# Performance work log

Hardware: AMD Instinct MI355X
Metric: run time of the kernel (lower is better)

## Reference

```python
import jax, jax.numpy as jnp
import numpy as np

G, NB, C, K, R, S = 5, 5, 64, 3, 8, 2   # n_groups, n_blocks, n_feats, kernel, reduction, scale
MOCO = 256


def setup_inputs() -> dict:
    key = jax.random.key(0)
    ks = iter(jax.random.split(key, 32))
    def rn(shape, s=0.02):
        return jax.random.normal(next(ks), shape, jnp.float32) * s
    return {
        "x": jax.random.normal(next(ks), (16, 3, 64, 64), jnp.float32),
        "k_v": jax.random.normal(next(ks), (16, MOCO), jnp.float32),
        "head_w": rn((C, 3, K, K)), "head_b": rn((C,)),
        "comp_w": rn((C, MOCO)),
        # DA_conv params, stacked over [group, block, which-of-2]
        "da_kw1": rn((G, NB, 2, C, C)),
        "da_kw2": rn((G, NB, 2, C * K * K, C)),
        "da_cw": rn((G, NB, 2, C, C)), "da_cb": rn((G, NB, 2, C)),
        "ca_w1": rn((G, NB, 2, C // R, C)), "ca_w2": rn((G, NB, 2, C, C // R)),
        # DAB plain 3x3 convs (conv1, conv2)
        "dab_cw": rn((G, NB, 2, C, C, K, K)), "dab_cb": rn((G, NB, 2, C)),
        # per-group tail conv, body tail conv, upsampler, final conv
        "grp_w": rn((G, C, C, K, K)), "grp_b": rn((G, C)),
        "body_w": rn((C, C, K, K)), "body_b": rn((C,)),
        "up_w": rn((C * S * S, C, K, K)), "up_b": rn((C * S * S,)),
        "tail_w": rn((3, C, K, K)), "tail_b": rn((3,)),
    }


def lrelu(x):
    return jax.nn.leaky_relu(x, 0.1)


def conv2d(x, w, b):
    p = (K - 1) // 2
    y = jax.lax.conv_general_dilated(x, w, (1, 1), [(p, p), (p, p)],
                                     dimension_numbers=("NCHW", "OIHW", "NCHW"))
    return y + b[None, :, None, None]


def da_conv(x, kv, kw1, kw2, cw, cb, caw1, caw2):
    # x: [B,C,H,W], kv: [B,C]
    B, Ch, H, W = x.shape
    # per-sample, per-channel dynamic KxK kernel (torch: groups=B*C depthwise conv)
    ker = (lrelu(kv @ kw1.T) @ kw2.T).reshape(B, Ch, K, K)
    p = (K - 1) // 2
    xp = jnp.pad(x, ((0, 0), (0, 0), (p, p), (p, p)))
    out = jnp.zeros_like(x)
    for i in range(K):
        for j in range(K):
            out = out + ker[:, :, i, j, None, None] * xp[:, :, i:i + H, j:j + W]
    out = lrelu(out)
    # 1x1 conv (with bias)
    out = jnp.einsum("bchw,oc->bohw", out, cw) + cb[None, :, None, None]
    # CA gate on kv (two bias-free 1x1 convs on 1x1 spatial == matmuls)
    att = jax.nn.sigmoid(lrelu(kv @ caw1.T) @ caw2.T)  # [B,C]
    return out + x * att[:, :, None, None]


def pixel_shuffle(t, r):
    B, Ct, H, W = t.shape
    c = Ct // (r * r)
    return t.reshape(B, c, r, r, H, W).transpose(0, 1, 4, 2, 5, 3).reshape(B, c, H * r, W * r)


def _forward(x, k_v, head_w, head_b, comp_w, da_kw1, da_kw2, da_cw, da_cb,
             ca_w1, ca_w2, dab_cw, dab_cb, grp_w, grp_b, body_w, body_b,
             up_w, up_b, tail_w, tail_b):
    kv = lrelu(k_v @ comp_w.T)            # compress: [B, C]
    x0 = conv2d(x, head_w, head_b)        # head
    res = x0
    for g in range(G):                    # DAGs
        gin = res
        for n in range(NB):               # DABs
            bin_ = res
            out = lrelu(da_conv(res, kv, da_kw1[g, n, 0], da_kw2[g, n, 0],
                                da_cw[g, n, 0], da_cb[g, n, 0], ca_w1[g, n, 0], ca_w2[g, n, 0]))
            out = lrelu(conv2d(out, dab_cw[g, n, 0], dab_cb[g, n, 0]))
            out = lrelu(da_conv(out, kv, da_kw1[g, n, 1], da_kw2[g, n, 1],
                                da_cw[g, n, 1], da_cb[g, n, 1], ca_w1[g, n, 1], ca_w2[g, n, 1]))
            res = conv2d(out, dab_cw[g, n, 1], dab_cb[g, n, 1]) + bin_
        res = conv2d(res, grp_w[g], grp_b[g]) + gin
    res = conv2d(res, body_w, body_b) + x0
    t = pixel_shuffle(conv2d(res, up_w, up_b), S)   # Upsampler (scale=2)
    return conv2d(t, tail_w, tail_b)


def reference(x, k_v, head_w, head_b, comp_w, da_kw1, da_kw2, da_cw, da_cb,
              ca_w1, ca_w2, dab_cw, dab_cb, grp_w, grp_b, body_w, body_b,
              up_w, up_b, tail_w, tail_b):
    return _forward(x, k_v, head_w, head_b, comp_w, da_kw1, da_kw2, da_cw, da_cb,
                    ca_w1, ca_w2, dab_cw, dab_cb, grp_w, grp_b, body_w, body_b,
                    up_w, up_b, tail_w, tail_b)
```

## Files before the change

### kernel.cpp

```cpp
#include <hip/hip_runtime.h>
#include <math.h>

#define DEV __device__ __forceinline__

DEV float lrelu_f(float v) { return v > 0.f ? v : 0.1f * v; }

DEV unsigned short f2bf(float f) {
    unsigned u = __builtin_bit_cast(unsigned, f);
    unsigned r = u + 0x7FFFu + ((u >> 16) & 1u);
    return (unsigned short)(r >> 16);
}

DEV float bf2f(unsigned short s) {
    return __builtin_bit_cast(float, (unsigned)s << 16);
}

typedef __attribute__((ext_vector_type(8))) short bh8;
typedef __attribute__((ext_vector_type(16))) float f16acc;

#define MFMA32(acc, a, b) acc = __builtin_amdgcn_mfma_f32_32x32x16_bf16(a, b, acc, 0, 0, 0)

__global__ void transpose_w(const float* __restrict__ src, float* __restrict__ dst,
                            int L, int O, int KK) {
    int idx = blockIdx.x * 256 + threadIdx.x;
    int tot = L * O * KK;
    if (idx >= tot) return;
    int l = idx / (O * KK);
    int r = idx - l * (O * KK);
    int o = r / KK;
    int k = r - o * KK;
    dst[((size_t)l * KK + k) * O + o] = src[idx];
}

__global__ void pack3x3(const float* __restrict__ src, unsigned short* __restrict__ dst, int L) {
    int idx = blockIdx.x * 256 + threadIdx.x;
    if (idx >= L * 4608) return;
    int l = idx / 4608;
    int r = idx - l * 4608;
    int c = r >> 7;
    int rr = r & 127;
    int nt = rr >> 6, lane = rr & 63;
    int o = nt * 32 + (lane & 31);
    int kg = lane >> 5;
    unsigned short v[8];
#pragma unroll
    for (int j = 0; j < 8; ++j) {
        int k = c * 16 + kg * 8 + j;
        int t = k >> 6, cin = k & 63;
        v[j] = f2bf(src[(((size_t)l * 64 + o) * 64 + cin) * 9 + t]);
    }
    uint4 u;
    u.x = v[0] | ((unsigned)v[1] << 16);
    u.y = v[2] | ((unsigned)v[3] << 16);
    u.z = v[4] | ((unsigned)v[5] << 16);
    u.w = v[6] | ((unsigned)v[7] << 16);
    *(uint4*)(dst + (size_t)idx * 8) = u;
}

__global__ void pack_da(const float* __restrict__ src, unsigned short* __restrict__ dst, int L) {
    int idx = blockIdx.x * 256 + threadIdx.x;
    if (idx >= L * 512) return;
    int l = idx >> 9;
    int r = idx & 511;
    int c = r >> 7;
    int rr = r & 127;
    int nt = rr >> 6, lane = rr & 63;
    int o = nt * 32 + (lane & 31);
    int kg = lane >> 5;
    unsigned short v[8];
#pragma unroll
    for (int j = 0; j < 8; ++j) {
        int cin = c * 16 + kg * 8 + j;
        v[j] = f2bf(src[((size_t)l * 64 + o) * 64 + cin]);
    }
    uint4 u;
    u.x = v[0] | ((unsigned)v[1] << 16);
    u.y = v[2] | ((unsigned)v[3] << 16);
    u.z = v[4] | ((unsigned)v[5] << 16);
    u.w = v[6] | ((unsigned)v[7] << 16);
    *(uint4*)(dst + (size_t)idx * 8) = u;
}

__global__ void pack_up(const float* __restrict__ src, unsigned short* __restrict__ dst) {
    int idx = blockIdx.x * 256 + threadIdx.x;
    if (idx >= 18432) return;
    int c = idx >> 9;
    int nt = (idx >> 6) & 7;
    int lane = idx & 63;
    int o = nt * 32 + (lane & 31);
    int kg = lane >> 5;
    unsigned short v[8];
#pragma unroll
    for (int j = 0; j < 8; ++j) {
        int k = c * 16 + kg * 8 + j;
        int t = k >> 6, cin = k & 63;
        v[j] = f2bf(src[((size_t)o * 64 + cin) * 9 + t]);
    }
    uint4 u;
    u.x = v[0] | ((unsigned)v[1] << 16);
    u.y = v[2] | ((unsigned)v[3] << 16);
    u.z = v[4] | ((unsigned)v[5] << 16);
    u.w = v[6] | ((unsigned)v[7] << 16);
    *(uint4*)(dst + (size_t)idx * 8) = u;
}

__global__ void pack_tail(const float* __restrict__ src, unsigned short* __restrict__ dst) {
    int idx = blockIdx.x * 256 + threadIdx.x;
    if (idx >= 2304) return;
    int c = idx >> 6;
    int lane = idx & 63;
    int o = lane & 31;
    int kg = lane >> 5;
    unsigned short v[8];
#pragma unroll
    for (int j = 0; j < 8; ++j) {
        int k = c * 16 + kg * 8 + j;
        int t = k >> 6, cin = k & 63;
        v[j] = (o < 3) ? f2bf(src[((size_t)o * 64 + cin) * 9 + t]) : (unsigned short)0;
    }
    uint4 u;
    u.x = v[0] | ((unsigned)v[1] << 16);
    u.y = v[2] | ((unsigned)v[3] << 16);
    u.z = v[4] | ((unsigned)v[5] << 16);
    u.w = v[6] | ((unsigned)v[7] << 16);
    *(uint4*)(dst + (size_t)idx * 8) = u;
}

__global__ void kv_kernel(const float* __restrict__ kvin, const float* __restrict__ comp_w,
                          float* __restrict__ kv) {
    int b = blockIdx.x, c = threadIdx.x;
    const float* a = kvin + b * 256;
    const float* w = comp_w + c * 256;
    float s = 0.f;
    for (int m = 0; m < 256; ++m) s += a[m] * w[m];
    kv[b * 64 + c] = lrelu_f(s);
}

__global__ void kerprep(const float* __restrict__ kv, const float* __restrict__ kw1,
                        const float* __restrict__ kw2, const float* __restrict__ caw1,
                        const float* __restrict__ caw2, float* __restrict__ ker_all,
                        float* __restrict__ att_all) {
    int l = blockIdx.x >> 4;
    int b = blockIdx.x & 15;
    int c = threadIdx.x;
    __shared__ float kvb[64];
    __shared__ float t1[64];
    __shared__ float a1[8];
    kvb[c] = kv[b * 64 + c];
    __syncthreads();
    {
        const float* w1 = kw1 + (size_t)l * 4096 + c * 64;
        float s = 0.f;
        for (int j = 0; j < 64; ++j) s += kvb[j] * w1[j];
        t1[c] = lrelu_f(s);
    }
    if (c < 8) {
        const float* cw1 = caw1 + (size_t)l * 512 + c * 64;
        float s = 0.f;
        for (int j = 0; j < 64; ++j) s += kvb[j] * cw1[j];
        a1[c] = lrelu_f(s);
    }
    __syncthreads();
    const float* w2 = kw2 + (size_t)l * 576 * 64;
    for (int t = 0; t < 9; ++t) {
        const float* row = w2 + (size_t)(c * 9 + t) * 64;
        float s = 0.f;
        for (int j = 0; j < 64; ++j) s += t1[j] * row[j];
        ker_all[(((size_t)l * 16 + b) * 9 + t) * 64 + c] = s;
    }
    {
        const float* c2 = caw2 + (size_t)l * 512 + c * 8;
        float s = 0.f;
        for (int r = 0; r < 8; ++r) s += a1[r] * c2[r];
        att_all[((size_t)l * 16 + b) * 64 + c] = 1.f / (1.f + expf(-s));
    }
}

__global__ __launch_bounds__(256) void head_conv(const float* __restrict__ x,
                                                 const float* __restrict__ wt,
                                                 const float* __restrict__ bias,
                                                 float* __restrict__ x0,
                                                 float* __restrict__ res,
                                                 unsigned short* __restrict__ resS) {
    int t = threadIdx.x;
    int co = t & 63, q = t >> 6;
    int bid = blockIdx.x;
    int b = bid >> 7;
    int rem = bid & 127;
    int y = rem >> 1;
    int xs = (rem & 1) * 32 + q * 8;

    float bv = bias[co];
    float acc[8];
#pragma unroll
    for (int p = 0; p < 8; ++p) acc[p] = bv;

    int coff[10];
    bool cok[10];
#pragma unroll
    for (int i = 0; i < 10; ++i) {
        int col = xs - 1 + i;
        cok[i] = (col >= 0) && (col < 64);
        coff[i] = cok[i] ? col : 0;
    }
    for (int cin = 0; cin < 3; ++cin) {
#pragma unroll
        for (int ky = 0; ky < 3; ++ky) {
            int row = y + ky - 1;
            bool rok = (row >= 0) && (row < 64);
            const float* rp = x + ((size_t)(b * 3 + cin) * 64 + (rok ? row : 0)) * 64;
            float v[10];
#pragma unroll
            for (int i = 0; i < 10; ++i) v[i] = (rok && cok[i]) ? rp[coff[i]] : 0.f;
            const float* wp = wt + ((cin * 3 + ky) * 3) * 64 + co;
            float w0 = wp[0], w1 = wp[64], w2 = wp[128];
#pragma unroll
            for (int p = 0; p < 8; ++p) acc[p] += w0 * v[p] + w1 * v[p + 1] + w2 * v[p + 2];
        }
    }
    size_t ob = (((size_t)b * 64 + y) * 64 + xs) * 64 + co;
#pragma unroll
    for (int p = 0; p < 8; ++p) {
        x0[ob + (size_t)p * 64] = acc[p];
        res[ob + (size_t)p * 64] = acc[p];
        resS[ob + (size_t)p * 64] = f2bf(acc[p]);
    }
}

__global__ __launch_bounds__(256, 2) void conv3x3_mfma(const unsigned short* __restrict__ in,
                                                       const unsigned short* __restrict__ wp,
                                                       const float* __restrict__ bias,
                                                       const float* __restrict__ residF,
                                                       float* __restrict__ outF,
                                                       unsigned short* __restrict__ outB,
                                                       int act) {
    __shared__ unsigned short sm[180 * 72];
    int tid = threadIdx.x;
    int bid = blockIdx.x;
    int b = bid >> 5;
    int rem = bid & 31;
    int ty = rem >> 2, tx = rem & 3;
    const unsigned short* inb = in + (size_t)b * 262144;

    int lane = tid & 63, w = tid >> 6;
    const unsigned short* bp = wp + (size_t)lane * 8;

    bh8 q0[6], q1[6];
#pragma unroll
    for (int i = 0; i < 6; ++i) {
        q0[i] = *(const bh8*)&bp[(size_t)i * 1024];
        q1[i] = *(const bh8*)&bp[(size_t)i * 1024 + 512];
    }

    for (int i = tid; i < 1440; i += 256) {
        int px = i >> 3, c8 = i & 7;
        int hy = px / 18, hx = px - hy * 18;
        int row = ty * 8 + hy - 1, col = tx * 16 + hx - 1;
        uint4 u = make_uint4(0u, 0u, 0u, 0u);
        if (row >= 0 && row < 64 && col >= 0 && col < 64)
            u = *(const uint4*)(inb + (((size_t)row * 64 + col) * 64 + c8 * 8));
        *(uint4*)&sm[px * 72 + c8 * 8] = u;
    }
    __syncthreads();

    int l31 = lane & 31, kg8 = (lane >> 5) * 8, hi = lane >> 5;
    int p0 = w * 32 + l31;
    int ly0 = p0 >> 4, lx0 = p0 & 15;

    f16acc a0 = {0,0,0,0,0,0,0,0,0,0,0,0,0,0,0,0};
    f16acc a1 = a0;

#pragma unroll
    for (int c = 0; c < 36; ++c) {
        int t = c >> 2, cc = c & 3;
        int tyt = t / 3, txt = t - tyt * 3;
        int base = ((ly0 + tyt) * 18 + lx0 + txt) * 72 + cc * 16 + kg8;
        bh8 A = *(const bh8*)&sm[base];
        bh8 B0 = q0[c % 6], B1 = q1[c % 6];
        if (c + 6 < 36) {
            q0[c % 6] = *(const bh8*)&bp[(size_t)(c + 6) * 1024];
            q1[c % 6] = *(const bh8*)&bp[(size_t)(c + 6) * 1024 + 512];
        }
        MFMA32(a0, A, B0);
        MFMA32(a1, A, B1);
    }

    float bias0 = bias[l31], bias1 = bias[32 + l31];
    size_t outb = (size_t)b * 262144;
#pragma unroll
    for (int r = 0; r < 16; ++r) {
        int rowm = (r & 3) + 8 * (r >> 2) + 4 * hi;
        int m = w * 32 + rowm;
        int gy = ty * 8 + (m >> 4), gx = tx * 16 + (m & 15);
        size_t i0 = outb + (((size_t)gy * 64 + gx) * 64);
        float v0 = a0[r] + bias0, v1 = a1[r] + bias1;
        if (residF) {
            v0 += residF[i0 + l31];
            v1 += residF[i0 + 32 + l31];
        }
        if (act) { v0 = lrelu_f(v0); v1 = lrelu_f(v1); }
        if (outF) {
            outF[i0 + l31] = v0;
            outF[i0 + 32 + l31] = v1;
        }
        if (outB) {
            outB[i0 + l31] = f2bf(v0);
            outB[i0 + 32 + l31] = f2bf(v1);
        }
    }
}

__global__ __launch_bounds__(256, 2) void dab_mfma(const unsigned short* __restrict__ in,
                                                   const unsigned short* __restrict__ wda,
                                                   const float* __restrict__ cb,
                                                   const float* __restrict__ kerT,
                                                   const float* __restrict__ attv,
                                                   const unsigned short* __restrict__ wconv,
                                                   const float* __restrict__ cbias,
                                                   const float* __restrict__ residF,
                                                   float* __restrict__ outF,
                                                   unsigned short* __restrict__ outB,
                                                   int act) {
    __shared__ unsigned short sin_[240 * 72];
    __shared__ unsigned short mid[192 * 72];
    int tid = threadIdx.x;
    int bid = blockIdx.x;
    int b = bid >> 5;
    int rem = bid & 31;
    int ty = rem >> 2, tx = rem & 3;
    const unsigned short* inb = in + (size_t)b * 262144;

    int lane = tid & 63, w = tid >> 6;
    int l31 = lane & 31, kg8 = (lane >> 5) * 8, hi = lane >> 5;

    bh8 dB0[4], dB1[4];
#pragma unroll
    for (int cc = 0; cc < 4; ++cc) {
        dB0[cc] = *(const bh8*)&wda[((size_t)(cc * 2 + 0) * 64 + lane) * 8];
        dB1[cc] = *(const bh8*)&wda[((size_t)(cc * 2 + 1) * 64 + lane) * 8];
    }

    for (int i = tid; i < 1920; i += 256) {
        int px = i >> 3, c8 = i & 7;
        int hy = px / 20, hx = px - hy * 20;
        int row = ty * 8 + hy - 2, col = tx * 16 + hx - 2;
        uint4 u = make_uint4(0u, 0u, 0u, 0u);
        if (row >= 0 && row < 64 && col >= 0 && col < 64)
            u = *(const uint4*)(inb + (((size_t)row * 64 + col) * 64 + c8 * 8));
        *(uint4*)&sin_[px * 72 + c8 * 8] = u;
    }
    __syncthreads();

    {
        int c2 = tid & 31, q = tid >> 5;
        const float* kb = kerT + (size_t)b * 576 + 2 * c2;
        float ka[9], kbv[9];
#pragma unroll
        for (int t = 0; t < 9; ++t) {
            ka[t] = kb[t * 64];
            kbv[t] = kb[t * 64 + 1];
        }
#pragma unroll
        for (int rr = 0; rr < 2; ++rr) {
            int my = (rr == 0) ? q : 8 + q;
            if (rr == 1 && q >= 2) break;
            float m0[18], m1[18];
#pragma unroll
            for (int xx = 0; xx < 18; ++xx) { m0[xx] = 0.f; m1[xx] = 0.f; }
#pragma unroll
            for (int ky = 0; ky < 3; ++ky) {
                int sr = my + ky;
                float va[20], vb[20];
#pragma unroll
                for (int i = 0; i < 20; ++i) {
                    unsigned u = *(const unsigned*)&sin_[(sr * 20 + i) * 72 + 2 * c2];
                    va[i] = bf2f((unsigned short)(u & 0xffffu));
                    vb[i] = bf2f((unsigned short)(u >> 16));
                }
                float k0a = ka[ky * 3], k1a = ka[ky * 3 + 1], k2a = ka[ky * 3 + 2];
                float k0b = kbv[ky * 3], k1b = kbv[ky * 3 + 1], k2b = kbv[ky * 3 + 2];
#pragma unroll
                for (int xx = 0; xx < 18; ++xx) {
                    m0[xx] += k0a * va[xx] + k1a * va[xx + 1] + k2a * va[xx + 2];
                    m1[xx] += k0b * vb[xx] + k1b * vb[xx + 1] + k2b * vb[xx + 2];
                }
            }
#pragma unroll
            for (int xx = 0; xx < 18; ++xx) {
                int px = my * 18 + xx;
                unsigned u = (unsigned)f2bf(lrelu_f(m0[xx])) |
                             ((unsigned)f2bf(lrelu_f(m1[xx])) << 16);
                *(unsigned*)&mid[px * 72 + 2 * c2] = u;
            }
        }
    }
    __syncthreads();

    {
        float cb0 = cb[l31], cb1 = cb[32 + l31];
        float at0 = attv[b * 64 + l31], at1 = attv[b * 64 + 32 + l31];
        for (int mt = w; mt < 6; mt += 4) {
            f16acc a0 = {0,0,0,0,0,0,0,0,0,0,0,0,0,0,0,0};
            f16acc a1 = a0;
#pragma unroll
            for (int cc = 0; cc < 4; ++cc) {
                bh8 A = *(const bh8*)&mid[(mt * 32 + l31) * 72 + cc * 16 + kg8];
                MFMA32(a0, A, dB0[cc]);
                MFMA32(a1, A, dB1[cc]);
            }
#pragma unroll
            for (int r = 0; r < 16; ++r) {
                int rowm = (r & 3) + 8 * (r >> 2) + 4 * hi;
                int px = mt * 32 + rowm;
                if (px < 180) {
                    int my = px / 18, mx = px - my * 18;
                    int gy = ty * 8 + my - 1, gx = tx * 16 + mx - 1;
                    bool ok = (gy >= 0) && (gy < 64) && (gx >= 0) && (gx < 64);
                    int spx = (my + 1) * 20 + (mx + 1);
                    float i0v = bf2f(sin_[spx * 72 + l31]);
                    float i1v = bf2f(sin_[spx * 72 + 32 + l31]);
                    float v0 = lrelu_f(a0[r] + cb0 + i0v * at0);
                    float v1 = lrelu_f(a1[r] + cb1 + i1v * at1);
                    mid[px * 72 + l31] = ok ? f2bf(v0) : (unsigned short)0;
                    mid[px * 72 + 32 + l31] = ok ? f2bf(v1) : (unsigned short)0;
                }
            }
        }
    }

    const unsigned short* bp = wconv + (size_t)lane * 8;
    bh8 q0[6], q1[6];
#pragma unroll
    for (int i = 0; i < 6; ++i) {
        q0[i] = *(const bh8*)&bp[(size_t)i * 1024];
        q1[i] = *(const bh8*)&bp[(size_t)i * 1024 + 512];
    }
    __syncthreads();

    int p0 = w * 32 + l31;
    int ly0 = p0 >> 4, lx0 = p0 & 15;

    f16acc c0 = {0,0,0,0,0,0,0,0,0,0,0,0,0,0,0,0};
    f16acc c1 = c0;

#pragma unroll
    for (int c = 0; c < 36; ++c) {
        int t = c >> 2, cc = c & 3;
        int tyt = t / 3, txt = t - tyt * 3;
        int base = ((ly0 + tyt) * 18 + lx0 + txt) * 72 + cc * 16 + kg8;
        bh8 A = *(const bh8*)&mid[base];
        bh8 B0 = q0[c % 6], B1 = q1[c % 6];
        if (c + 6 < 36) {
            q0[c % 6] = *(const bh8*)&bp[(size_t)(c + 6) * 1024];
            q1[c % 6] = *(const bh8*)&bp[(size_t)(c + 6) * 1024 + 512];
        }
        MFMA32(c0, A, B0);
        MFMA32(c1, A, B1);
    }

    float bias0 = cbias[l31], bias1 = cbias[32 + l31];
    size_t outb = (size_t)b * 262144;
#pragma unroll
    for (int r = 0; r < 16; ++r) {
        int rowm = (r & 3) + 8 * (r >> 2) + 4 * hi;
        int m = w * 32 + rowm;
        int gy = ty * 8 + (m >> 4), gx = tx * 16 + (m & 15);
        size_t i0 = outb + (((size_t)gy * 64 + gx) * 64);
        float v0 = c0[r] + bias0, v1 = c1[r] + bias1;
        if (residF) {
            v0 += residF[i0 + l31];
            v1 += residF[i0 + 32 + l31];
        }
        if (act) { v0 = lrelu_f(v0); v1 = lrelu_f(v1); }
        if (outF) {
            outF[i0 + l31] = v0;
            outF[i0 + 32 + l31] = v1;
        }
        if (outB) {
            outB[i0 + l31] = f2bf(v0);
            outB[i0 + 32 + l31] = f2bf(v1);
        }
    }
}

__global__ __launch_bounds__(256, 2) void up_mfma(const unsigned short* __restrict__ in,
                                                  const unsigned short* __restrict__ wp,
                                                  const float* __restrict__ bias,
                                                  unsigned short* __restrict__ shuf) {
    __shared__ unsigned short sm[100 * 72];
    int tid = threadIdx.x;
    int bid = blockIdx.x;
    int b = bid >> 6;
    int t6 = bid & 63;
    int ty = t6 >> 3, tx = t6 & 7;
    const unsigned short* inb = in + (size_t)b * 262144;

    int lane = tid & 63, w = tid >> 6;
    const unsigned short* bp = wp + (size_t)(w * 2) * 512 + (size_t)lane * 8;

    bh8 q0[4], q1[4];
#pragma unroll
    for (int i = 0; i < 4; ++i) {
        q0[i] = *(const bh8*)&bp[(size_t)i * 4096];
        q1[i] = *(const bh8*)&bp[(size_t)i * 4096 + 512];
    }

    for (int i = tid; i < 800; i += 256) {
        int px = i >> 3, c8 = i & 7;
        int hy = px / 10, hx = px - hy * 10;
        int row = ty * 8 + hy - 1, col = tx * 8 + hx - 1;
        uint4 u = make_uint4(0u, 0u, 0u, 0u);
        if (row >= 0 && row < 64 && col >= 0 && col < 64)
            u = *(const uint4*)(inb + (((size_t)row * 64 + col) * 64 + c8 * 8));
        *(uint4*)&sm[px * 72 + c8 * 8] = u;
    }
    __syncthreads();

    int l31 = lane & 31, kg8 = (lane >> 5) * 8, hi = lane >> 5;
    int ly0 = l31 >> 3, lx0 = l31 & 7;

    f16acc a00 = {0,0,0,0,0,0,0,0,0,0,0,0,0,0,0,0};
    f16acc a01 = a00, a10 = a00, a11 = a00;

#pragma unroll
    for (int c = 0; c < 36; ++c) {
        int t = c >> 2, cc = c & 3;
        int tyt = t / 3, txt = t - tyt * 3;
        int base0 = ((ly0 + tyt) * 10 + lx0 + txt) * 72 + cc * 16 + kg8;
        int base1 = base0 + 2880;
        bh8 A0 = *(const bh8*)&sm[base0];
        bh8 A1 = *(const bh8*)&sm[base1];
        bh8 B0 = q0[c % 4], B1 = q1[c % 4];
        if (c + 4 < 36) {
            q0[c % 4] = *(const bh8*)&bp[(size_t)(c + 4) * 4096];
            q1[c % 4] = *(const bh8*)&bp[(size_t)(c + 4) * 4096 + 512];
        }
        MFMA32(a00, A0, B0);
        MFMA32(a01, A0, B1);
        MFMA32(a10, A1, B0);
        MFMA32(a11, A1, B1);
    }

    int co0 = w * 64 + l31, co1 = co0 + 32;
    float bias0 = bias[co0], bias1 = bias[co1];
    int ch0 = co0 >> 2, r10 = (co0 >> 1) & 1, r20 = co0 & 1;
    int ch1 = co1 >> 2, r11 = (co1 >> 1) & 1, r21 = co1 & 1;
#pragma unroll
    for (int r = 0; r < 16; ++r) {
        int rowm = (r & 3) + 8 * (r >> 2) + 4 * hi;
#pragma unroll
        for (int mt = 0; mt < 2; ++mt) {
            int m = mt * 32 + rowm;
            int y = ty * 8 + (m >> 3), x = tx * 8 + (m & 7);
            float va = (mt == 0) ? a00[r] : a10[r];
            float vb = (mt == 0) ? a01[r] : a11[r];
            shuf[(((size_t)b * 128 + 2 * y + r10) * 128 + 2 * x + r20) * 64 + ch0] = f2bf(va + bias0);
            shuf[(((size_t)b * 128 + 2 * y + r11) * 128 + 2 * x + r21) * 64 + ch1] = f2bf(vb + bias1);
        }
    }
}

__global__ __launch_bounds__(256) void tail_mfma(const unsigned short* __restrict__ shuf,
                                                 const unsigned short* __restrict__ wp,
                                                 const float* __restrict__ bias,
                                                 float* __restrict__ outp) {
    __shared__ unsigned short sm[324 * 72];
    int tid = threadIdx.x;
    int bid = blockIdx.x;
    int b = bid >> 6;
    int rem = bid & 63;
    int ty = rem >> 3, tx = rem & 7;
    const unsigned short* sb = shuf + (size_t)b * 128 * 128 * 64;

    for (int i = tid; i < 2592; i += 256) {
        int px = i >> 3, c8 = i & 7;
        int hy = px / 18, hx = px - hy * 18;
        int row = ty * 16 + hy - 1, col = tx * 16 + hx - 1;
        uint4 u = make_uint4(0u, 0u, 0u, 0u);
        if (row >= 0 && row < 128 && col >= 0 && col < 128)
            u = *(const uint4*)(sb + (((size_t)row * 128 + col) * 64 + c8 * 8));
        *(uint4*)&sm[px * 72 + c8 * 8] = u;
    }
    __syncthreads();

    int lane = tid & 63, w = tid >> 6;
    int l31 = lane & 31, kg8 = (lane >> 5) * 8, hi = lane >> 5;
    int mbase = w * 64;
    int p0 = mbase + l31;
    int ly0 = p0 >> 4, lx0 = p0 & 15;

    f16acc a0 = {0,0,0,0,0,0,0,0,0,0,0,0,0,0,0,0};
    f16acc a1 = a0;

#pragma unroll
    for (int t = 0; t < 9; ++t) {
        int tyt = t / 3, txt = t - tyt * 3;
        int base0 = ((ly0 + tyt) * 18 + lx0 + txt) * 72 + kg8;
        int base1 = base0 + 2592;
#pragma unroll
        for (int cc = 0; cc < 4; ++cc) {
            int c = t * 4 + cc;
            bh8 A0 = *(const bh8*)&sm[base0 + cc * 16];
            bh8 A1 = *(const bh8*)&sm[base1 + cc * 16];
            bh8 B = *(const bh8*)&wp[((size_t)c * 64 + lane) * 8];
            MFMA32(a0, A0, B);
            MFMA32(a1, A1, B);
        }
    }

    if (l31 < 3) {
        float bv = bias[l31];
        size_t ob = ((size_t)b * 3 + l31) * 16384;
#pragma unroll
        for (int r = 0; r < 16; ++r) {
            int rowm = (r & 3) + 8 * (r >> 2) + 4 * hi;
            int m0 = mbase + rowm;
            int gy0 = ty * 16 + (m0 >> 4), gx0 = tx * 16 + (m0 & 15);
            outp[ob + (size_t)gy0 * 128 + gx0] = a0[r] + bv;
            int m1 = m0 + 32;
            int gy1 = ty * 16 + (m1 >> 4), gx1 = tx * 16 + (m1 & 15);
            outp[ob + (size_t)gy1 * 128 + gx1] = a1[r] + bv;
        }
    }
}

extern "C" void kernel_launch(void* const* d_in, const int* in_sizes, int n_in,
                              void* d_out, int out_size, void* d_ws, size_t ws_size,
                              hipStream_t stream) {
    const float* x      = (const float*)d_in[0];
    const float* k_v    = (const float*)d_in[1];
    const float* head_w = (const float*)d_in[2];
    const float* head_b = (const float*)d_in[3];
    const float* comp_w = (const float*)d_in[4];
    const float* da_kw1 = (const float*)d_in[5];
    const float* da_kw2 = (const float*)d_in[6];
    const float* da_cw  = (const float*)d_in[7];
    const float* da_cb  = (const float*)d_in[8];
    const float* ca_w1  = (const float*)d_in[9];
    const float* ca_w2  = (const float*)d_in[10];
    const float* dab_cw = (const float*)d_in[11];
    const float* dab_cb = (const float*)d_in[12];
    const float* grp_w  = (const float*)d_in[13];
    const float* grp_b  = (const float*)d_in[14];
    const float* body_w = (const float*)d_in[15];
    const float* body_b = (const float*)d_in[16];
    const float* up_w   = (const float*)d_in[17];
    const float* up_b   = (const float*)d_in[18];
    const float* tail_w = (const float*)d_in[19];
    const float* tail_b = (const float*)d_in[20];

    char* base = (char*)d_ws;
    auto alloc = [&](size_t bytes) -> char* {
        char* p = base;
        base += (bytes + 255) & ~(size_t)255;
        return p;
    };
    unsigned short* wp_dab  = (unsigned short*)alloc((size_t)50 * 36864 * 2);
    unsigned short* wp_grp  = (unsigned short*)alloc((size_t)5 * 36864 * 2);
    unsigned short* wp_body = (unsigned short*)alloc((size_t)36864 * 2);
    unsigned short* wp_up   = (unsigned short*)alloc((size_t)147456 * 2);
    unsigned short* wp_da   = (unsigned short*)alloc((size_t)50 * 4096 * 2);
    unsigned short* wp_tail = (unsigned short*)alloc((size_t)18432 * 2);
    float* wT_head = (float*)alloc(1728 * 4);
    float* kvbuf   = (float*)alloc(1024 * 4);
    float* ker_all = (float*)alloc((size_t)460800 * 4);
    float* att_all = (float*)alloc((size_t)51200 * 4);
    const size_t ACT = (size_t)16 * 64 * 64 * 64;
    float* x0 = (float*)alloc(ACT * 4);
    float* rA = (float*)alloc(ACT * 4);
    float* rB = (float*)alloc(ACT * 4);
    float* rC = (float*)alloc(ACT * 4);
    unsigned short* sA = (unsigned short*)alloc(ACT * 2);
    unsigned short* sB = (unsigned short*)alloc(ACT * 2);
    unsigned short* sC = (unsigned short*)alloc(ACT * 2);
    unsigned short* t1 = (unsigned short*)alloc(ACT * 2);
    unsigned short* shuf = (unsigned short*)alloc((size_t)16 * 128 * 128 * 64 * 2);

    pack3x3<<<900, 256, 0, stream>>>(dab_cw, wp_dab, 50);
    pack3x3<<<90, 256, 0, stream>>>(grp_w, wp_grp, 5);
    pack3x3<<<18, 256, 0, stream>>>(body_w, wp_body, 1);
    pack_da<<<100, 256, 0, stream>>>(da_cw, wp_da, 50);
    pack_up<<<72, 256, 0, stream>>>(up_w, wp_up);
    pack_tail<<<9, 256, 0, stream>>>(tail_w, wp_tail);
    transpose_w<<<7, 256, 0, stream>>>(head_w, wT_head, 1, 64, 27);

    kv_kernel<<<16, 64, 0, stream>>>(k_v, comp_w, kvbuf);
    kerprep<<<800, 64, 0, stream>>>(kvbuf, da_kw1, da_kw2, ca_w1, ca_w2, ker_all, att_all);

    head_conv<<<2048, 256, 0, stream>>>(x, wT_head, head_b, x0, rA, sA);

    for (int g = 0; g < 5; ++g) {
        float* curF = rA;
        unsigned short* curS = sA;
        for (int n = 0; n < 5; ++n) {
            int l0 = (g * 5 + n) * 2, l1 = l0 + 1;
            dab_mfma<<<512, 256, 0, stream>>>(curS,
                                              wp_da + (size_t)l0 * 4096,
                                              da_cb + (size_t)l0 * 64,
                                              ker_all + (size_t)l0 * 9216,
                                              att_all + (size_t)l0 * 1024,
                                              wp_dab + (size_t)l0 * 36864,
                                              dab_cb + (size_t)l0 * 64,
                                              nullptr, nullptr, t1, 1);
            float* outF = (curF == rB) ? rC : rB;
            unsigned short* outS = (curS == sB) ? sC : sB;
            dab_mfma<<<512, 256, 0, stream>>>(t1,
                                              wp_da + (size_t)l1 * 4096,
                                              da_cb + (size_t)l1 * 64,
                                              ker_all + (size_t)l1 * 9216,
                                              att_all + (size_t)l1 * 1024,
                                              wp_dab + (size_t)l1 * 36864,
                                              dab_cb + (size_t)l1 * 64,
                                              curF, outF, outS, 0);
            curF = outF;
            curS = outS;
        }
        conv3x3_mfma<<<512, 256, 0, stream>>>(curS, wp_grp + (size_t)g * 36864,
                                              grp_b + (size_t)g * 64, rA, rC, sC, 0);
        float* tf = rA; rA = rC; rC = tf;
        unsigned short* ts = sA; sA = sC; sC = ts;
    }
    conv3x3_mfma<<<512, 256, 0, stream>>>(sA, wp_body, body_b, x0, nullptr, t1, 0);

    up_mfma<<<1024, 256, 0, stream>>>(t1, wp_up, up_b, shuf);
    tail_mfma<<<1024, 256, 0, stream>>>(shuf, wp_tail, tail_b, (float*)d_out);
}
```

Baseline: 1.537 ms.

## Shrink conv and DAB spatial tiles to 8x8 and split output channels across waves

Switches the 3x3 conv and fused DAB kernels from 8x16 spatial tiles to 8x8 tiles. Each wave now computes one 32-channel half for 32 pixels, instead of both halves for 32 pixels. The grid doubles to 1024 blocks, LDS use shrinks, and launch bounds rise to 4 blocks per SM, aiming for better occupancy and load balance. The cost is a larger share of halo overhead: the depthwise stage recomputes 10x10 mid tiles for 64 outputs instead of 18x10 for 128. Input loads and depthwise work per output pixel therefore go up.

```diff
diff --git a/kernel.cpp b/kernel.cpp
--- a/kernel.cpp
+++ b/kernel.cpp
@@ -227,35 +227,33 @@
     }
 }
 
-__global__ __launch_bounds__(256, 2) void conv3x3_mfma(const unsigned short* __restrict__ in,
+__global__ __launch_bounds__(256, 4) void conv3x3_mfma(const unsigned short* __restrict__ in,
                                                        const unsigned short* __restrict__ wp,
                                                        const float* __restrict__ bias,
                                                        const float* __restrict__ residF,
                                                        float* __restrict__ outF,
                                                        unsigned short* __restrict__ outB,
                                                        int act) {
-    __shared__ unsigned short sm[180 * 72];
+    __shared__ unsigned short sm[100 * 72];
     int tid = threadIdx.x;
     int bid = blockIdx.x;
-    int b = bid >> 5;
-    int rem = bid & 31;
-    int ty = rem >> 2, tx = rem & 3;
+    int b = bid >> 6;
+    int rem = bid & 63;
+    int ty = rem >> 3, tx = rem & 7;
     const unsigned short* inb = in + (size_t)b * 262144;
 
     int lane = tid & 63, w = tid >> 6;
-    const unsigned short* bp = wp + (size_t)lane * 8;
-
-    bh8 q0[6], q1[6];
-#pragma unroll
-    for (int i = 0; i < 6; ++i) {
-        q0[i] = *(const bh8*)&bp[(size_t)i * 1024];
-        q1[i] = *(const bh8*)&bp[(size_t)i * 1024 + 512];
-    }
-
-    for (int i = tid; i < 1440; i += 256) {
+    int mp = w & 1, nt = w >> 1;
+    const unsigned short* bp = wp + (size_t)nt * 512 + (size_t)lane * 8;
+
+    bh8 q[6];
+#pragma unroll
+    for (int i = 0; i < 6; ++i) q[i] = *(const bh8*)&bp[(size_t)i * 1024];
+
+    for (int i = tid; i < 800; i += 256) {
         int px = i >> 3, c8 = i & 7;
-        int hy = px / 18, hx = px - hy * 18;
-        int row = ty * 8 + hy - 1, col = tx * 16 + hx - 1;
+        int hy = px / 10, hx = px - hy * 10;
+        int row = ty * 8 + hy - 1, col = tx * 8 + hx - 1;
         uint4 u = make_uint4(0u, 0u, 0u, 0u);
         if (row >= 0 && row < 64 && col >= 0 && col < 64)
             u = *(const uint4*)(inb + (((size_t)row * 64 + col) * 64 + c8 * 8));
@@ -264,53 +262,40 @@
     __syncthreads();
 
     int l31 = lane & 31, kg8 = (lane >> 5) * 8, hi = lane >> 5;
-    int p0 = w * 32 + l31;
-    int ly0 = p0 >> 4, lx0 = p0 & 15;
+    int p0 = mp * 32 + l31;
+    int ly0 = p0 >> 3, lx0 = p0 & 7;
 
     f16acc a0 = {0,0,0,0,0,0,0,0,0,0,0,0,0,0,0,0};
-    f16acc a1 = a0;
 
 #pragma unroll
     for (int c = 0; c < 36; ++c) {
         int t = c >> 2, cc = c & 3;
         int tyt = t / 3, txt = t - tyt * 3;
-        int base = ((ly0 + tyt) * 18 + lx0 + txt) * 72 + cc * 16 + kg8;
+        int base = ((ly0 + tyt) * 10 + lx0 + txt) * 72 + cc * 16 + kg8;
         bh8 A = *(const bh8*)&sm[base];
-        bh8 B0 = q0[c % 6], B1 = q1[c % 6];
-        if (c + 6 < 36) {
-            q0[c % 6] = *(const bh8*)&bp[(size_t)(c + 6) * 1024];
-            q1[c % 6] = *(const bh8*)&bp[(size_t)(c + 6) * 1024 + 512];
-        }
-        MFMA32(a0, A, B0);
-        MFMA32(a1, A, B1);
-    }
-
-    float bias0 = bias[l31], bias1 = bias[32 + l31];
+        bh8 B = q[c % 6];
+        if (c + 6 < 36) q[c % 6] = *(const bh8*)&bp[(size_t)(c + 6) * 1024];
+        MFMA32(a0, A, B);
+    }
+
+    float bv = bias[nt * 32 + l31];
+    int ch = nt * 32 + l31;
     size_t outb = (size_t)b * 262144;
 #pragma unroll
     for (int r = 0; r < 16; ++r) {
         int rowm = (r & 3) + 8 * (r >> 2) + 4 * hi;
-        int m = w * 32 + rowm;
-        int gy = ty * 8 + (m >> 4), gx = tx * 16 + (m & 15);
-        size_t i0 = outb + (((size_t)gy * 64 + gx) * 64);
-        float v0 = a0[r] + bias0, v1 = a1[r] + bias1;
-        if (residF) {
-            v0 += residF[i0 + l31];
-            v1 += residF[i0 + 32 + l31];
-        }
-        if (act) { v0 = lrelu_f(v0); v1 = lrelu_f(v1); }
-        if (outF) {
-            outF[i0 + l31] = v0;
-            outF[i0 + 32 + l31] = v1;
-        }
-        if (outB) {
-            outB[i0 + l31] = f2bf(v0);
-            outB[i0 + 32 + l31] = f2bf(v1);
-        }
-    }
-}
-
-__global__ __launch_bounds__(256, 2) void dab_mfma(const unsigned short* __restrict__ in,
+        int m = mp * 32 + rowm;
+        int gy = ty * 8 + (m >> 3), gx = tx * 8 + (m & 7);
+        size_t i0 = outb + (((size_t)gy * 64 + gx) * 64) + ch;
+        float v0 = a0[r] + bv;
+        if (residF) v0 += residF[i0];
+        if (act) v0 = lrelu_f(v0);
+        if (outF) outF[i0] = v0;
+        if (outB) outB[i0] = f2bf(v0);
+    }
+}
+
+__global__ __launch_bounds__(256, 4) void dab_mfma(const unsigned short* __restrict__ in,
                                                    const unsigned short* __restrict__ wda,
                                                    const float* __restrict__ cb,
                                                    const float* __restrict__ kerT,
@@ -321,13 +306,13 @@
                                                    float* __restrict__ outF,
                                                    unsigned short* __restrict__ outB,
                                                    int act) {
-    __shared__ unsigned short sin_[240 * 72];
-    __shared__ unsigned short mid[192 * 72];
+    __shared__ unsigned short sin_[144 * 72];
+    __shared__ unsigned short mid[128 * 72];
     int tid = threadIdx.x;
     int bid = blockIdx.x;
-    int b = bid >> 5;
-    int rem = bid & 31;
-    int ty = rem >> 2, tx = rem & 3;
+    int b = bid >> 6;
+    int rem = bid & 63;
+    int ty = rem >> 3, tx = rem & 7;
     const unsigned short* inb = in + (size_t)b * 262144;
 
     int lane = tid & 63, w = tid >> 6;
@@ -340,10 +325,10 @@
         dB1[cc] = *(const bh8*)&wda[((size_t)(cc * 2 + 1) * 64 + lane) * 8];
     }
 
-    for (int i = tid; i < 1920; i += 256) {
+    for (int i = tid; i < 1152; i += 256) {
         int px = i >> 3, c8 = i & 7;
-        int hy = px / 20, hx = px - hy * 20;
-        int row = ty * 8 + hy - 2, col = tx * 16 + hx - 2;
+        int hy = px / 12, hx = px - hy * 12;
+        int row = ty * 8 + hy - 2, col = tx * 8 + hx - 2;
         uint4 u = make_uint4(0u, 0u, 0u, 0u);
         if (row >= 0 && row < 64 && col >= 0 && col < 64)
             u = *(const uint4*)(inb + (((size_t)row * 64 + col) * 64 + c8 * 8));
@@ -352,7 +337,7 @@
     __syncthreads();
 
     {
-        int c2 = tid & 31, q = tid >> 5;
+        int c2 = tid & 31, qi = tid >> 5;
         const float* kb = kerT + (size_t)b * 576 + 2 * c2;
         float ka[9], kbv[9];
 #pragma unroll
@@ -362,32 +347,32 @@
         }
 #pragma unroll
         for (int rr = 0; rr < 2; ++rr) {
-            int my = (rr == 0) ? q : 8 + q;
-            if (rr == 1 && q >= 2) break;
-            float m0[18], m1[18];
-#pragma unroll
-            for (int xx = 0; xx < 18; ++xx) { m0[xx] = 0.f; m1[xx] = 0.f; }
+            int my = (rr == 0) ? qi : 8 + qi;
+            if (rr == 1 && qi >= 2) break;
+            float m0[10], m1[10];
+#pragma unroll
+            for (int xx = 0; xx < 10; ++xx) { m0[xx] = 0.f; m1[xx] = 0.f; }
 #pragma unroll
             for (int ky = 0; ky < 3; ++ky) {
                 int sr = my + ky;
-                float va[20], vb[20];
-#pragma unroll
-                for (int i = 0; i < 20; ++i) {
-                    unsigned u = *(const unsigned*)&sin_[(sr * 20 + i) * 72 + 2 * c2];
+                float va[12], vb[12];
+#pragma unroll
+                for (int i = 0; i < 12; ++i) {
+                    unsigned u = *(const unsigned*)&sin_[(sr * 12 + i) * 72 + 2 * c2];
                     va[i] = bf2f((unsigned short)(u & 0xffffu));
                     vb[i] = bf2f((unsigned short)(u >> 16));
                 }
                 float k0a = ka[ky * 3], k1a = ka[ky * 3 + 1], k2a = ka[ky * 3 + 2];
                 float k0b = kbv[ky * 3], k1b = kbv[ky * 3 + 1], k2b = kbv[ky * 3 + 2];
 #pragma unroll
-                for (int xx = 0; xx < 18; ++xx) {
+                for (int xx = 0; xx < 10; ++xx) {
                     m0[xx] += k0a * va[xx] + k1a * va[xx + 1] + k2a * va[xx + 2];
                     m1[xx] += k0b * vb[xx] + k1b * vb[xx + 1] + k2b * vb[xx + 2];
                 }
             }
 #pragma unroll
-            for (int xx = 0; xx < 18; ++xx) {
-                int px = my * 18 + xx;
+            for (int xx = 0; xx < 10; ++xx) {
+                int px = my * 10 + xx;
                 unsigned u = (unsigned)f2bf(lrelu_f(m0[xx])) |
                              ((unsigned)f2bf(lrelu_f(m1[xx])) << 16);
                 *(unsigned*)&mid[px * 72 + 2 * c2] = u;
@@ -399,7 +384,7 @@
     {
         float cb0 = cb[l31], cb1 = cb[32 + l31];
         float at0 = attv[b * 64 + l31], at1 = attv[b * 64 + 32 + l31];
-        for (int mt = w; mt < 6; mt += 4) {
+        for (int mt = w; mt < 4; mt += 4) {
             f16acc a0 = {0,0,0,0,0,0,0,0,0,0,0,0,0,0,0,0};
             f16acc a1 = a0;
 #pragma unroll
@@ -412,11 +397,11 @@
             for (int r = 0; r < 16; ++r) {
                 int rowm = (r & 3) + 8 * (r >> 2) + 4 * hi;
                 int px = mt * 32 + rowm;
-                if (px < 180) {
-                    int my = px / 18, mx = px - my * 18;
-                    int gy = ty * 8 + my - 1, gx = tx * 16 + mx - 1;
+                if (px < 100) {
+                    int my = px / 10, mx = px - my * 10;
+                    int gy = ty * 8 + my - 1, gx = tx * 8 + mx - 1;
                     bool ok = (gy >= 0) && (gy < 64) && (gx >= 0) && (gx < 64);
-                    int spx = (my + 1) * 20 + (mx + 1);
+                    int spx = (my + 1) * 12 + (mx + 1);
                     float i0v = bf2f(sin_[spx * 72 + l31]);
                     float i1v = bf2f(sin_[spx * 72 + 32 + l31]);
                     float v0 = lrelu_f(a0[r] + cb0 + i0v * at0);
@@ -428,58 +413,43 @@
         }
     }
 
-    const unsigned short* bp = wconv + (size_t)lane * 8;
-    bh8 q0[6], q1[6];
-#pragma unroll
-    for (int i = 0; i < 6; ++i) {
-        q0[i] = *(const bh8*)&bp[(size_t)i * 1024];
-        q1[i] = *(const bh8*)&bp[(size_t)i * 1024 + 512];
-    }
-    __syncthreads();
-
-    int p0 = w * 32 + l31;
-    int ly0 = p0 >> 4, lx0 = p0 & 15;
+    int mp = w & 1, nt = w >> 1;
+    const unsigned short* bp = wconv + (size_t)nt * 512 + (size_t)lane * 8;
+    bh8 q[6];
+#pragma unroll
+    for (int i = 0; i < 6; ++i) q[i] = *(const bh8*)&bp[(size_t)i * 1024];
+    __syncthreads();
+
+    int p0 = mp * 32 + l31;
+    int ly0 = p0 >> 3, lx0 = p0 & 7;
 
     f16acc c0 = {0,0,0,0,0,0,0,0,0,0,0,0,0,0,0,0};
-    f16acc c1 = c0;
 
 #pragma unroll
     for (int c = 0; c < 36; ++c) {
         int t = c >> 2, cc = c & 3;
         int tyt = t / 3, txt = t - tyt * 3;
-        int base = ((ly0 + tyt) * 18 + lx0 + txt) * 72 + cc * 16 + kg8;
+        int base = ((ly0 + tyt) * 10 + lx0 + txt) * 72 + cc * 16 + kg8;
         bh8 A = *(const bh8*)&mid[base];
-        bh8 B0 = q0[c % 6], B1 = q1[c % 6];
-        if (c + 6 < 36) {
-            q0[c % 6] = *(const bh8*)&bp[(size_t)(c + 6) * 1024];
-            q1[c % 6] = *(const bh8*)&bp[(size_t)(c + 6) * 1024 + 512];
-        }
-        MFMA32(c0, A, B0);
-        MFMA32(c1, A, B1);
-    }
-
-    float bias0 = cbias[l31], bias1 = cbias[32 + l31];
+        bh8 B = q[c % 6];
+        if (c + 6 < 36) q[c % 6] = *(const bh8*)&bp[(size_t)(c + 6) * 1024];
+        MFMA32(c0, A, B);
+    }
+
+    float bv = cbias[nt * 32 + l31];
+    int ch = nt * 32 + l31;
     size_t outb = (size_t)b * 262144;
 #pragma unroll
     for (int r = 0; r < 16; ++r) {
         int rowm = (r & 3) + 8 * (r >> 2) + 4 * hi;
-        int m = w * 32 + rowm;
-        int gy = ty * 8 + (m >> 4), gx = tx * 16 + (m & 15);
-        size_t i0 = outb + (((size_t)gy * 64 + gx) * 64);
-        float v0 = c0[r] + bias0, v1 = c1[r] + bias1;
-        if (residF) {
-            v0 += residF[i0 + l31];
-            v1 += residF[i0 + 32 + l31];
-        }
-        if (act) { v0 = lrelu_f(v0); v1 = lrelu_f(v1); }
-        if (outF) {
-            outF[i0 + l31] = v0;
-            outF[i0 + 32 + l31] = v1;
-        }
-        if (outB) {
-            outB[i0 + l31] = f2bf(v0);
-            outB[i0 + 32 + l31] = f2bf(v1);
-        }
+        int m = mp * 32 + rowm;
+        int gy = ty * 8 + (m >> 3), gx = tx * 8 + (m & 7);
+        size_t i0 = outb + (((size_t)gy * 64 + gx) * 64) + ch;
+        float v0 = c0[r] + bv;
+        if (residF) v0 += residF[i0];
+        if (act) v0 = lrelu_f(v0);
+        if (outF) outF[i0] = v0;
+        if (outB) outB[i0] = f2bf(v0);
     }
 }
 
@@ -694,33 +664,33 @@
         unsigned short* curS = sA;
         for (int n = 0; n < 5; ++n) {
             int l0 = (g * 5 + n) * 2, l1 = l0 + 1;
-            dab_mfma<<<512, 256, 0, stream>>>(curS,
-                                              wp_da + (size_t)l0 * 4096,
-                                              da_cb + (size_t)l0 * 64,
-                                              ker_all + (size_t)l0 * 9216,
-                                              att_all + (size_t)l0 * 1024,
-                                              wp_dab + (size_t)l0 * 36864,
-                                              dab_cb + (size_t)l0 * 64,
-                                              nullptr, nullptr, t1, 1);
+            dab_mfma<<<1024, 256, 0, stream>>>(curS,
+                                               wp_da + (size_t)l0 * 4096,
+                                               da_cb + (size_t)l0 * 64,
+                                               ker_all + (size_t)l0 * 9216,
+                                               att_all + (size_t)l0 * 1024,
+                                               wp_dab + (size_t)l0 * 36864,
+                                               dab_cb + (size_t)l0 * 64,
+                                               nullptr, nullptr, t1, 1);
             float* outF = (curF == rB) ? rC : rB;
             unsigned short* outS = (curS == sB) ? sC : sB;
-            dab_mfma<<<512, 256, 0, stream>>>(t1,
-                                              wp_da + (size_t)l1 * 4096,
-                                              da_cb + (size_t)l1 * 64,
-                                              ker_all + (size_t)l1 * 9216,
-                                              att_all + (size_t)l1 * 1024,
-                                              wp_dab + (size_t)l1 * 36864,
-                                              dab_cb + (size_t)l1 * 64,
-                                              curF, outF, outS, 0);
+            dab_mfma<<<1024, 256, 0, stream>>>(t1,
+                                               wp_da + (size_t)l1 * 4096,
+                                               da_cb + (size_t)l1 * 64,
+                                               ker_all + (size_t)l1 * 9216,
+                                               att_all + (size_t)l1 * 1024,
+                                               wp_dab + (size_t)l1 * 36864,
+                                               dab_cb + (size_t)l1 * 64,
+                                               curF, outF, outS, 0);
             curF = outF;
             curS = outS;
         }
-        conv3x3_mfma<<<512, 256, 0, stream>>>(curS, wp_grp + (size_t)g * 36864,
-                                              grp_b + (size_t)g * 64, rA, rC, sC, 0);
+        conv3x3_mfma<<<1024, 256, 0, stream>>>(curS, wp_grp + (size_t)g * 36864,
+                                               grp_b + (size_t)g * 64, rA, rC, sC, 0);
         float* tf = rA; rA = rC; rC = tf;
         unsigned short* ts = sA; sA = sC; sC = ts;
     }
-    conv3x3_mfma<<<512, 256, 0, stream>>>(sA, wp_body, body_b, x0, nullptr, t1, 0);
+    conv3x3_mfma<<<1024, 256, 0, stream>>>(sA, wp_body, body_b, x0, nullptr, t1, 0);
 
     up_mfma<<<1024, 256, 0, stream>>>(t1, wp_up, up_b, shuf);
     tail_mfma<<<1024, 256, 0, stream>>>(shuf, wp_tail, tail_b, (float*)d_out);
```

Result: slower. 1.913 ms (+24.5%).
